# Kernel optimization log

Measured on AMD Instinct MI355X. Metric: run time of the kernel, lower is better.

The kernel has to match this reference:

```python
import jax, jax.numpy as jnp
import numpy as np

# ---- problem sizes ----
CNO = 10000        # constant_no
PAD = 10001        # padding_idx (also used as the 'variable' marker in queries)
KS = max(CNO, PAD) + 2   # key_scale / pack_base = 10003
N_PRED = 128
F = 2_000_000
B = 200_000


def _build_segment_index(keys: np.ndarray, max_key: int):
    """numpy replica of torch _build_segment_index: (order, starts, lens)."""
    order = np.argsort(keys, kind='stable')
    uniq, counts = np.unique(keys, return_counts=True)  # unique keys, sorted
    starts = np.zeros(max_key, dtype=np.int64)
    lens = np.zeros(max_key, dtype=np.int64)
    cum = np.cumsum(counts)
    starts[uniq] = cum - counts
    lens[uniq] = counts
    return order, starts, lens


def setup_inputs() -> dict:
    rng = np.random.default_rng(0)
    # facts: [F,3] (pred, arg0, arg1), constants in [1, CNO]
    fp = rng.integers(0, N_PRED, F)
    fa0 = rng.integers(1, CNO + 1, F)
    fa1 = rng.integers(1, CNO + 1, F)
    # FactIndex.__init__ sorts facts by packed hash before building indices
    hashes = (fp.astype(np.int64) * KS + fa0) * KS + fa1
    h_order = np.argsort(hashes, kind='stable')
    fp, fa0, fa1 = fp[h_order], fa0[h_order], fa1[h_order]
    # three segment indexes: (pred,arg0), (pred,arg1), pred-only
    k0 = fp.astype(np.int64) * KS + fa0
    k1 = fp.astype(np.int64) * KS + fa1
    o0, s0, l0 = _build_segment_index(k0, int(k0.max()) + 1)
    o1, s1, l1 = _build_segment_index(k1, int(k1.max()) + 1)
    op, sp, lp = _build_segment_index(fp.astype(np.int64), int(fp.max()) + 1)
    # queries: 1/3 (pred,const,var), 1/3 (pred,var,const), 1/3 (pred,var,var)
    qp = rng.integers(0, N_PRED, B)
    pattern = rng.integers(0, 3, B)
    c0 = rng.integers(1, CNO + 1, B)
    c1 = rng.integers(1, CNO + 1, B)
    qa0 = np.where(pattern == 0, c0, PAD)
    qa1 = np.where(pattern == 1, c1, PAD)
    query_atoms = np.stack([qp, qa0, qa1], axis=1)
    ja = lambda a: jnp.asarray(a, dtype=jnp.int32)
    return {
        'query_atoms': ja(query_atoms),
        'a0_order': ja(o0), 'a0_starts': ja(s0), 'a0_lens': ja(l0),
        'a1_order': ja(o1), 'a1_starts': ja(s1), 'a1_lens': ja(l1),
        'p_order': ja(op), 'p_starts': ja(sp), 'p_lens': ja(lp),
        'max_results': 64,
    }


def reference(query_atoms, a0_order, a0_starts, a0_lens,
              a1_order, a1_starts, a1_lens,
              p_order, p_starts, p_lens, max_results):
    B = query_atoms.shape[0]
    F = a0_order.shape[0]
    clamp_max = max(F - 1, 0)
    preds = query_atoms[:, 0]
    a0 = query_atoms[:, 1]
    a1 = query_atoms[:, 2]
    is_c0 = (a0 <= CNO) & (a0 != PAD)
    is_c1 = (a1 <= CNO) & (a1 != PAD)
    offsets = jnp.arange(max_results, dtype=jnp.int32)[None, :]  # [1,K]

    def _lookup(order, starts, lens, keys, is_const):
        safe = jnp.clip(keys, 0, starts.shape[0] - 1)
        left = starts[safe]                                  # [B]
        cnt = jnp.minimum(lens[safe], max_results)           # [B]
        idx = jnp.clip(left[:, None] + offsets, 0, clamp_max)  # [B,K]
        v = (offsets < cnt[:, None]) & is_const[:, None]
        return order[idx], v

    fi0, v0 = _lookup(a0_order, a0_starts, a0_lens, preds * KS + a0, is_c0)
    fi1, v1 = _lookup(a1_order, a1_starts, a1_lens, preds * KS + a1, is_c1)
    use0 = is_c0[:, None]
    fact_idx = jnp.where(use0, fi0, fi1)
    valid = jnp.where(use0, v0, v1)
    # pred-only fallback when both args are variables
    both_var = (~is_c0) & (~is_c1) & (preds != PAD)
    fip, vp = _lookup(p_order, p_starts, p_lens, preds, both_var)
    bv = both_var[:, None]
    fact_idx = jnp.where(bv, fip, fact_idx)
    valid = jnp.where(bv, vp, valid)
    return fact_idx, valid
```

## Files before the change

kernel.cpp:

```cpp
#include <hip/hip_runtime.h>

#define CNO_C 10000
#define PAD_C 10001
#define KS_C  10003

template <bool MR64>
__global__ __launch_bounds__(256) void akfi_vec4(
    const int* __restrict__ qa,
    const int* __restrict__ o0, const int* __restrict__ s0, const int* __restrict__ l0,
    const int* __restrict__ o1, const int* __restrict__ s1, const int* __restrict__ l1,
    const int* __restrict__ op, const int* __restrict__ sp, const int* __restrict__ lp,
    int n0, int n1, int npred,
    int F, int B, int mr,
    int* __restrict__ out_idx,
    int* __restrict__ out_valid)
{
    long long t = (long long)blockIdx.x * blockDim.x + threadIdx.x;
    int per_q = mr >> 2;
    long long total = (long long)B * per_q;
    if (t >= total) return;

    int q, j4;
    if (MR64) { q = (int)(t >> 4); j4 = (int)((t & 15) << 2); }
    else      { q = (int)(t / per_q); j4 = (int)(t % per_q) << 2; }

    int p  = qa[q * 3 + 0];
    int a0 = qa[q * 3 + 1];
    int a1 = qa[q * 3 + 2];

    bool is_c0 = (a0 <= CNO_C) && (a0 != PAD_C);
    bool is_c1 = (a1 <= CNO_C) && (a1 != PAD_C);
    bool both  = (!is_c0) && (!is_c1) && (p != PAD_C);

    const int* order;
    const int* starts;
    const int* lens;
    int key, nsz;
    bool isc;
    if (is_c0)      { order = o0; starts = s0; lens = l0; key = p * KS_C + a0; nsz = n0;    isc = true;  }
    else if (both)  { order = op; starts = sp; lens = lp; key = p;             nsz = npred; isc = true;  }
    else            { order = o1; starts = s1; lens = l1; key = p * KS_C + a1; nsz = n1;    isc = is_c1; }

    int safe = key;
    if (safe < 0)       safe = 0;
    if (safe > nsz - 1) safe = nsz - 1;

    int left = starts[safe];
    int cnt  = lens[safe];
    if (cnt > mr) cnt = mr;

    int idx0 = left + j4;
    int f0, f1, f2, f3;
    if (idx0 >= 0 && idx0 + 3 <= F - 1) {
        f0 = order[idx0];
        f1 = order[idx0 + 1];
        f2 = order[idx0 + 2];
        f3 = order[idx0 + 3];
    } else {
        int i0 = min(max(idx0,     0), F - 1);
        int i1 = min(max(idx0 + 1, 0), F - 1);
        int i2 = min(max(idx0 + 2, 0), F - 1);
        int i3 = min(max(idx0 + 3, 0), F - 1);
        f0 = order[i0]; f1 = order[i1]; f2 = order[i2]; f3 = order[i3];
    }

    int4 fv = make_int4(f0, f1, f2, f3);
    int4 vv = make_int4(
        (isc && (j4     < cnt)) ? 1 : 0,
        (isc && (j4 + 1 < cnt)) ? 1 : 0,
        (isc && (j4 + 2 < cnt)) ? 1 : 0,
        (isc && (j4 + 3 < cnt)) ? 1 : 0);

    long long ob = (long long)q * mr + j4;
    *reinterpret_cast<int4*>(out_idx + ob)   = fv;
    *reinterpret_cast<int4*>(out_valid + ob) = vv;
}

__global__ __launch_bounds__(256) void akfi_scalar(
    const int* __restrict__ qa,
    const int* __restrict__ o0, const int* __restrict__ s0, const int* __restrict__ l0,
    const int* __restrict__ o1, const int* __restrict__ s1, const int* __restrict__ l1,
    const int* __restrict__ op, const int* __restrict__ sp, const int* __restrict__ lp,
    int n0, int n1, int npred,
    int F, int B, int mr,
    int* __restrict__ out_idx,
    int* __restrict__ out_valid)
{
    long long t = (long long)blockIdx.x * blockDim.x + threadIdx.x;
    long long total = (long long)B * (long long)mr;
    if (t >= total) return;
    int q = (int)(t / mr), j = (int)(t % mr);

    int p  = qa[q * 3 + 0];
    int a0 = qa[q * 3 + 1];
    int a1 = qa[q * 3 + 2];
    bool is_c0 = (a0 <= CNO_C) && (a0 != PAD_C);
    bool is_c1 = (a1 <= CNO_C) && (a1 != PAD_C);
    bool both  = (!is_c0) && (!is_c1) && (p != PAD_C);

    const int* order; const int* starts; const int* lens;
    int key, nsz; bool isc;
    if (is_c0)      { order = o0; starts = s0; lens = l0; key = p * KS_C + a0; nsz = n0;    isc = true;  }
    else if (both)  { order = op; starts = sp; lens = lp; key = p;             nsz = npred; isc = true;  }
    else            { order = o1; starts = s1; lens = l1; key = p * KS_C + a1; nsz = n1;    isc = is_c1; }

    int safe = min(max(key, 0), nsz - 1);
    int left = starts[safe];
    int cnt  = min(lens[safe], mr);
    int idx  = min(max(left + j, 0), F - 1);

    long long ob = (long long)q * mr + j;
    out_idx[ob]   = order[idx];
    out_valid[ob] = (isc && j < cnt) ? 1 : 0;
}

extern "C" void kernel_launch(void* const* d_in, const int* in_sizes, int n_in,
                              void* d_out, int out_size, void* d_ws, size_t ws_size,
                              hipStream_t stream) {
    const int* qa = (const int*)d_in[0];
    const int* o0 = (const int*)d_in[1];
    const int* s0 = (const int*)d_in[2];
    const int* l0 = (const int*)d_in[3];
    const int* o1 = (const int*)d_in[4];
    const int* s1 = (const int*)d_in[5];
    const int* l1 = (const int*)d_in[6];
    const int* op = (const int*)d_in[7];
    const int* sp = (const int*)d_in[8];
    const int* lp = (const int*)d_in[9];
    int B  = in_sizes[0] / 3;
    int F  = in_sizes[1];
    int n0 = in_sizes[2];
    int n1 = in_sizes[5];
    int npred = in_sizes[8];
    int mr = out_size / (2 * B);

    int* out_idx   = (int*)d_out;
    int* out_valid = (int*)d_out + (long long)B * mr;

    int block = 256;
    if ((mr & 3) == 0) {
        long long total = (long long)B * (mr >> 2);
        int blocks = (int)((total + block - 1) / block);
        if (mr == 64) {
            akfi_vec4<true><<<blocks, block, 0, stream>>>(
                qa, o0, s0, l0, o1, s1, l1, op, sp, lp,
                n0, n1, npred, F, B, mr, out_idx, out_valid);
        } else {
            akfi_vec4<false><<<blocks, block, 0, stream>>>(
                qa, o0, s0, l0, o1, s1, l1, op, sp, lp,
                n0, n1, npred, F, B, mr, out_idx, out_valid);
        }
    } else {
        long long total = (long long)B * (long long)mr;
        int blocks = (int)((total + block - 1) / block);
        akfi_scalar<<<blocks, block, 0, stream>>>(
            qa, o0, s0, l0, o1, s1, l1, op, sp, lp,
            n0, n1, npred, F, B, mr, out_idx, out_valid);
    }
}
```

Measured before the change: 31.77 us.

## Compute per-query segment descriptors once per block in shared memory for mr=64

Adds a specialised kernel for max_results=64 where each block handles 256 queries. Each thread first loads one query, resolves its table and reads its start and length, then stores a descriptor in shared memory. After a barrier, threads loop over 16 queries each, writing four consecutive outputs per query. This removes the 16x redundant query and start/length loads per query in exchange for a block barrier, a serial loop and fewer launched blocks.

Result: slower. 35.00 us (+10.2%).

```diff
diff --git a/kernel.cpp b/kernel.cpp
--- a/kernel.cpp
+++ b/kernel.cpp
@@ -4,7 +4,88 @@
 #define PAD_C 10001
 #define KS_C  10003
 
-template <bool MR64>
+__global__ __launch_bounds__(256) void akfi_block64(
+    const int* __restrict__ qa,
+    const int* __restrict__ o0, const int* __restrict__ s0, const int* __restrict__ l0,
+    const int* __restrict__ o1, const int* __restrict__ s1, const int* __restrict__ l1,
+    const int* __restrict__ op, const int* __restrict__ sp, const int* __restrict__ lp,
+    int n0, int n1, int npred,
+    int F, int B,
+    int* __restrict__ out_idx,
+    int* __restrict__ out_valid)
+{
+    __shared__ int4 desc[256];
+
+    const int tid   = threadIdx.x;
+    const int qbase = blockIdx.x << 8;
+
+    {
+        int q = qbase + tid;
+        if (q < B) {
+            int p  = qa[q * 3 + 0];
+            int a0 = qa[q * 3 + 1];
+            int a1 = qa[q * 3 + 2];
+
+            bool is_c0 = (a0 <= CNO_C) && (a0 != PAD_C);
+            bool is_c1 = (a1 <= CNO_C) && (a1 != PAD_C);
+            bool both  = (!is_c0) && (!is_c1) && (p != PAD_C);
+
+            const int* starts; const int* lens;
+            int key, nsz, tbl; bool isc;
+            if (is_c0)      { starts = s0; lens = l0; key = p * KS_C + a0; nsz = n0;    isc = true;  tbl = 0; }
+            else if (both)  { starts = sp; lens = lp; key = p;             nsz = npred; isc = true;  tbl = 1; }
+            else            { starts = s1; lens = l1; key = p * KS_C + a1; nsz = n1;    isc = is_c1; tbl = 2; }
+
+            int safe = min(max(key, 0), nsz - 1);
+            int left = starts[safe];
+            int cnt  = min(lens[safe], 64);
+            int cnt_eff = isc ? cnt : 0;
+
+            desc[tid] = make_int4(left, cnt_eff, tbl, 0);
+        }
+    }
+    __syncthreads();
+
+    const int lq  = tid >> 4;
+    const int j4  = (tid & 15) << 2;
+    const int Fm1 = F - 1;
+
+#pragma unroll 4
+    for (int i = 0; i < 16; ++i) {
+        int qq = lq + (i << 4);
+        int q  = qbase + qq;
+        if (q >= B) continue;
+
+        int4 d = desc[qq];
+        const int* order = (d.z == 0) ? o0 : (d.z == 1) ? op : o1;
+
+        int idx0 = d.x + j4;
+        int f0, f1, f2, f3;
+        if (idx0 >= 0 && idx0 + 3 <= Fm1) {
+            f0 = order[idx0];
+            f1 = order[idx0 + 1];
+            f2 = order[idx0 + 2];
+            f3 = order[idx0 + 3];
+        } else {
+            f0 = order[min(max(idx0,     0), Fm1)];
+            f1 = order[min(max(idx0 + 1, 0), Fm1)];
+            f2 = order[min(max(idx0 + 2, 0), Fm1)];
+            f3 = order[min(max(idx0 + 3, 0), Fm1)];
+        }
+
+        int cnt = d.y;
+        int4 fv = make_int4(f0, f1, f2, f3);
+        int4 vv = make_int4(j4 < cnt ? 1 : 0,
+                            j4 + 1 < cnt ? 1 : 0,
+                            j4 + 2 < cnt ? 1 : 0,
+                            j4 + 3 < cnt ? 1 : 0);
+
+        long long ob = ((long long)q << 6) + j4;
+        *reinterpret_cast<int4*>(out_idx + ob)   = fv;
+        *reinterpret_cast<int4*>(out_valid + ob) = vv;
+    }
+}
+
 __global__ __launch_bounds__(256) void akfi_vec4(
     const int* __restrict__ qa,
     const int* __restrict__ o0, const int* __restrict__ s0, const int* __restrict__ l0,
@@ -20,57 +101,41 @@
     long long total = (long long)B * per_q;
     if (t >= total) return;
 
-    int q, j4;
-    if (MR64) { q = (int)(t >> 4); j4 = (int)((t & 15) << 2); }
-    else      { q = (int)(t / per_q); j4 = (int)(t % per_q) << 2; }
+    int q = (int)(t / per_q), j4 = (int)(t % per_q) << 2;
 
     int p  = qa[q * 3 + 0];
     int a0 = qa[q * 3 + 1];
     int a1 = qa[q * 3 + 2];
-
     bool is_c0 = (a0 <= CNO_C) && (a0 != PAD_C);
     bool is_c1 = (a1 <= CNO_C) && (a1 != PAD_C);
     bool both  = (!is_c0) && (!is_c1) && (p != PAD_C);
 
-    const int* order;
-    const int* starts;
-    const int* lens;
-    int key, nsz;
-    bool isc;
+    const int* order; const int* starts; const int* lens;
+    int key, nsz; bool isc;
     if (is_c0)      { order = o0; starts = s0; lens = l0; key = p * KS_C + a0; nsz = n0;    isc = true;  }
     else if (both)  { order = op; starts = sp; lens = lp; key = p;             nsz = npred; isc = true;  }
     else            { order = o1; starts = s1; lens = l1; key = p * KS_C + a1; nsz = n1;    isc = is_c1; }
 
-    int safe = key;
-    if (safe < 0)       safe = 0;
-    if (safe > nsz - 1) safe = nsz - 1;
-
+    int safe = min(max(key, 0), nsz - 1);
     int left = starts[safe];
-    int cnt  = lens[safe];
-    if (cnt > mr) cnt = mr;
+    int cnt  = min(lens[safe], mr);
+    if (!isc) cnt = 0;
+    int Fm1 = F - 1;
 
     int idx0 = left + j4;
     int f0, f1, f2, f3;
-    if (idx0 >= 0 && idx0 + 3 <= F - 1) {
-        f0 = order[idx0];
-        f1 = order[idx0 + 1];
-        f2 = order[idx0 + 2];
-        f3 = order[idx0 + 3];
+    if (idx0 >= 0 && idx0 + 3 <= Fm1) {
+        f0 = order[idx0]; f1 = order[idx0 + 1]; f2 = order[idx0 + 2]; f3 = order[idx0 + 3];
     } else {
-        int i0 = min(max(idx0,     0), F - 1);
-        int i1 = min(max(idx0 + 1, 0), F - 1);
-        int i2 = min(max(idx0 + 2, 0), F - 1);
-        int i3 = min(max(idx0 + 3, 0), F - 1);
-        f0 = order[i0]; f1 = order[i1]; f2 = order[i2]; f3 = order[i3];
+        f0 = order[min(max(idx0,     0), Fm1)];
+        f1 = order[min(max(idx0 + 1, 0), Fm1)];
+        f2 = order[min(max(idx0 + 2, 0), Fm1)];
+        f3 = order[min(max(idx0 + 3, 0), Fm1)];
     }
 
     int4 fv = make_int4(f0, f1, f2, f3);
-    int4 vv = make_int4(
-        (isc && (j4     < cnt)) ? 1 : 0,
-        (isc && (j4 + 1 < cnt)) ? 1 : 0,
-        (isc && (j4 + 2 < cnt)) ? 1 : 0,
-        (isc && (j4 + 3 < cnt)) ? 1 : 0);
-
+    int4 vv = make_int4(j4 < cnt ? 1 : 0, j4 + 1 < cnt ? 1 : 0,
+                        j4 + 2 < cnt ? 1 : 0, j4 + 3 < cnt ? 1 : 0);
     long long ob = (long long)q * mr + j4;
     *reinterpret_cast<int4*>(out_idx + ob)   = fv;
     *reinterpret_cast<int4*>(out_valid + ob) = vv;
@@ -138,18 +203,17 @@
     int* out_valid = (int*)d_out + (long long)B * mr;
 
     int block = 256;
-    if ((mr & 3) == 0) {
+    if (mr == 64) {
+        int blocks = (B + 255) / 256;
+        akfi_block64<<<blocks, block, 0, stream>>>(
+            qa, o0, s0, l0, o1, s1, l1, op, sp, lp,
+            n0, n1, npred, F, B, out_idx, out_valid);
+    } else if ((mr & 3) == 0) {
         long long total = (long long)B * (mr >> 2);
         int blocks = (int)((total + block - 1) / block);
-        if (mr == 64) {
-            akfi_vec4<true><<<blocks, block, 0, stream>>>(
-                qa, o0, s0, l0, o1, s1, l1, op, sp, lp,
-                n0, n1, npred, F, B, mr, out_idx, out_valid);
-        } else {
-            akfi_vec4<false><<<blocks, block, 0, stream>>>(
-                qa, o0, s0, l0, o1, s1, l1, op, sp, lp,
-                n0, n1, npred, F, B, mr, out_idx, out_valid);
-        }
+        akfi_vec4<<<blocks, block, 0, stream>>>(
+            qa, o0, s0, l0, o1, s1, l1, op, sp, lp,
+            n0, n1, npred, F, B, mr, out_idx, out_valid);
     } else {
         long long total = (long long)B * (long long)mr;
         int blocks = (int)((total + block - 1) / block);
```
